# Kernel tuning notes

Measured on AMD Instinct MI355X. Metric: run time of the kernel, lower is better.

The kernel has to match this reference:

```python
import jax, jax.numpy as jnp
import numpy as np

B = 1024       # repertoires (batch)
TCR = 100      # instances (TCRs) per repertoire
FEAT = 15      # feature_num (conv in_channels)
AA = 24        # aa_num (sequence length)
KS = [2, 3, 4, 5, 6, 7]
FN = [3, 3, 3, 2, 2, 1]
NINP = 14      # sum(FN)
EPS = 1e-5     # BatchNorm eps


def sparsemax(z):
    # z: (B, K); sparsemax along axis 1 (Martins & Astudillo 2016)
    K = z.shape[1]
    zs = -jnp.sort(-z, axis=1)               # descending sort
    cs = jnp.cumsum(zs, axis=1)
    k = jnp.arange(1, K + 1, dtype=z.dtype)
    support = 1.0 + k * zs > cs              # (B, K) bool
    ksel = jnp.sum(support, axis=1, keepdims=True).astype(jnp.int32)  # support size
    tau = (jnp.take_along_axis(cs, ksel - 1, axis=1) - 1.0) / ksel.astype(z.dtype)
    return jnp.maximum(z - tau, 0.0)


def setup_inputs() -> dict:
    key = jax.random.key(0)
    ks = jax.random.split(key, 12)
    inp = {"x": jax.random.normal(ks[0], (B, TCR, FEAT, AA), dtype=jnp.float32)}
    for i, (h, f) in enumerate(zip(KS, FN)):
        inp[f"cw{i}"] = jax.random.normal(ks[1 + i], (f, FEAT, h), dtype=jnp.float32) * 0.1
        inp[f"cb{i}"] = jnp.zeros((f,), dtype=jnp.float32)
    inp["fc1_w"] = jax.random.normal(ks[7], (NINP, NINP), dtype=jnp.float32) * 0.2
    inp["fc1_b"] = jnp.zeros((NINP,), dtype=jnp.float32)
    inp["waout_w"] = jax.random.normal(ks[8], (1, NINP), dtype=jnp.float32) * 0.2
    inp["decf_w"] = jax.random.normal(ks[9], (NINP, NINP), dtype=jnp.float32) * 0.2
    inp["decf_b"] = jnp.zeros((NINP,), dtype=jnp.float32)
    inp["bn_g"] = jnp.ones((NINP,), dtype=jnp.float32)
    inp["bn_b"] = jnp.zeros((NINP,), dtype=jnp.float32)
    inp["decs_w"] = jax.random.normal(ks[10], (2, NINP), dtype=jnp.float32) * 0.2
    inp["decs_b"] = jnp.zeros((2,), dtype=jnp.float32)
    return inp


def reference(x, cw0, cb0, cw1, cb1, cw2, cb2, cw3, cb3, cw4, cb4, cw5, cb5,
              fc1_w, fc1_b, waout_w, decf_w, decf_b, bn_g, bn_b, decs_w, decs_b):
    xf = x.reshape(-1, FEAT, AA)  # (B*TCR, 15, 24)
    feats = []
    for w, b in ((cw0, cb0), (cw1, cb1), (cw2, cb2), (cw3, cb3), (cw4, cb4), (cw5, cb5)):
        y = jax.lax.conv_general_dilated(xf, w, (1,), 'VALID',
                                         dimension_numbers=('NCH', 'OIH', 'NCH'))
        y = jax.nn.relu(y + b[None, :, None])
        feats.append(jnp.max(y, axis=-1))  # AdaptiveMaxPool1d(1): global max over length
    out = jnp.concatenate(feats, axis=1).reshape(-1, TCR, NINP)  # (B, TCR, 14)
    # fclayer1 + dropout(eval=identity) + relu; applied per-instance so the
    # torch (TCR, B, .) transpose is equivalent to working in (B, TCR, .)
    h = jax.nn.relu(out @ fc1_w.T + fc1_b)                       # (B, TCR, 14)
    attw = sparsemax(h @ waout_w[0])                             # (B, TCR)
    pooled = jnp.einsum('bt,btd->bd', attw, h)                   # bmm(attw[:,None,:], h)
    z = pooled @ decf_w.T + decf_b                               # decoder_f
    mu = jnp.mean(z, axis=0)                                     # BatchNorm1d (batch stats)
    var = jnp.var(z, axis=0)
    z = jax.nn.relu((z - mu) / jnp.sqrt(var + EPS) * bn_g + bn_b)
    logits = z @ decs_w.T + decs_b                               # decoder_s -> (B, 2)
    return logits, attw
```

## Files before the change

### kernel.cpp

```cpp
#include <hip/hip_runtime.h>

typedef unsigned int  u32;
typedef unsigned short u16;

__device__ __forceinline__ float bf2f(u16 u){
    return __uint_as_float(((u32)u) << 16);
}
__device__ __forceinline__ u16 f2bf(float f){
    u32 x = __float_as_uint(f);
    x += 0x7fffu + ((x >> 16) & 1u);
    return (u16)(x >> 16);
}
__device__ __forceinline__ float ldany(const void* p, int i, bool bf){
    return bf ? bf2f(((const u16*)p)[i]) : ((const float*)p)[i];
}

#define B_      1024
#define TCR_    100
#define NINST   (B_*TCR_)

#define OFF_WL     0
#define OFF_CB     840
#define OFF_FC1W   854
#define OFF_FC1B   1050
#define OFF_WA     1064
#define OFF_DECFW  1078
#define OFF_DECFB  1274
#define OFF_BNG    1288
#define OFF_BNB    1302
#define OFF_DECSW  1316
#define OFF_DECSB  1344
#define NPARAM     1346

__global__ __launch_bounds__(256) void k_pack(
    const void* cw0, const void* cb0, const void* cw1, const void* cb1,
    const void* cw2, const void* cb2, const void* cw3, const void* cb3,
    const void* cw4, const void* cb4, const void* cw5, const void* cb5,
    const void* fc1_w, const void* fc1_b, const void* waout,
    const void* decf_w, const void* decf_b,
    const void* bn_g, const void* bn_b,
    const void* decs_w, const void* decs_b,
    float* __restrict__ wsP)
{
    const int tid = threadIdx.x;
    const bool bf = (((const u16*)bn_g)[0] == 0x3F80u);

    for (int widx = tid; widx < 840; widx += 256){
        float val;
        if (widx < 90)      { int e = widx;       int c=e/6,  rr=e-c*6,  ff=rr/2, j=rr-ff*2; val=ldany(cw0,(ff*15+c)*2+j,bf); }
        else if (widx < 225){ int e = widx - 90;  int c=e/9,  rr=e-c*9,  ff=rr/3, j=rr-ff*3; val=ldany(cw1,(ff*15+c)*3+j,bf); }
        else if (widx < 405){ int e = widx - 225; int c=e/12, rr=e-c*12, ff=rr/4, j=rr-ff*4; val=ldany(cw2,(ff*15+c)*4+j,bf); }
        else if (widx < 555){ int e = widx - 405; int c=e/10, rr=e-c*10, ff=rr/5, j=rr-ff*5; val=ldany(cw3,(ff*15+c)*5+j,bf); }
        else if (widx < 735){ int e = widx - 555; int c=e/12, rr=e-c*12, ff=rr/6, j=rr-ff*6; val=ldany(cw4,(ff*15+c)*6+j,bf); }
        else                { int e = widx - 735; int c=e/7,  j=e-c*7;                        val=ldany(cw5,c*7+j,bf); }
        wsP[OFF_WL + widx] = val;
    }
    for (int i = tid; i < 14; i += 256){
        float bv;
        if (i < 3)       bv = ldany(cb0, i, bf);
        else if (i < 6)  bv = ldany(cb1, i - 3, bf);
        else if (i < 9)  bv = ldany(cb2, i - 6, bf);
        else if (i < 11) bv = ldany(cb3, i - 9, bf);
        else if (i < 13) bv = ldany(cb4, i - 11, bf);
        else             bv = ldany(cb5, 0, bf);
        wsP[OFF_CB    + i] = bv;
        wsP[OFF_FC1B  + i] = ldany(fc1_b,  i, bf);
        wsP[OFF_WA    + i] = ldany(waout,  i, bf);
        wsP[OFF_DECFB + i] = ldany(decf_b, i, bf);
        wsP[OFF_BNG   + i] = ldany(bn_g,   i, bf);
        wsP[OFF_BNB   + i] = ldany(bn_b,   i, bf);
    }
    for (int i = tid; i < 196; i += 256){
        wsP[OFF_FC1W  + i] = ldany(fc1_w,  i, bf);
        wsP[OFF_DECFW + i] = ldany(decf_w, i, bf);
    }
    for (int i = tid; i < 28; i += 256) wsP[OFF_DECSW + i] = ldany(decs_w, i, bf);
    for (int i = tid; i < 2;  i += 256) wsP[OFF_DECSB + i] = ldany(decs_b, i, bf);
}

template<int H, int F, int WOFF, int C0, int C1>
__device__ __forceinline__ void conv_phase(const float* xsf, const float* pl,
                                           float (&acc)[3][23], int lane){
    for (int c = C0; c < C1; ++c){
        float xr[24];
        const float* row = xsf + ((c - C0) * 24) * 65 + lane;
        #pragma unroll
        for (int t = 0; t < 24; ++t) xr[t] = row[t * 65];
        float wv[F * H];
        #pragma unroll
        for (int k = 0; k < F * H; ++k) wv[k] = pl[WOFF + c * F * H + k];
        #pragma unroll
        for (int ff = 0; ff < F; ++ff)
            #pragma unroll
            for (int t = 0; t < 25 - H; ++t)
                #pragma unroll
                for (int j = 0; j < H; ++j)
                    acc[ff][t] = fmaf(wv[ff * H + j], xr[t + j], acc[ff][t]);
    }
}

template<int H, int F, int FB>
__device__ __forceinline__ void conv_epi(float (&acc)[3][23], const float* pl,
                                         float* feats, int lane){
    #pragma unroll
    for (int ff = 0; ff < F; ++ff){
        float m = acc[ff][0];
        #pragma unroll
        for (int t = 1; t < 25 - H; ++t) m = fmaxf(m, acc[ff][t]);
        feats[(FB + ff) * 64 + lane] = fmaxf(m + pl[OFF_CB + FB + ff], 0.0f);
    }
}

__global__ __launch_bounds__(384) void k_conv(
    const void* __restrict__ x, const float* __restrict__ wsP,
    const void* __restrict__ dt,
    float* __restrict__ hbuf, float* __restrict__ sbuf)
{
    __shared__ float xsf[192 * 65];
    __shared__ float pl[1078];
    __shared__ float feats[14 * 64];

    const int tid  = threadIdx.x;
    const int lane = tid & 63;
    const int wvid = tid >> 6;
    const bool bf  = (((const u16*)dt)[0] == 0x3F80u);
    const size_t ibase = (size_t)blockIdx.x * 64;

    for (int i = tid; i < 1078; i += 384) pl[i] = wsP[i];

    float acc[3][23];
    #pragma unroll
    for (int ff = 0; ff < 3; ++ff)
        #pragma unroll
        for (int t = 0; t < 23; ++t) acc[ff][t] = 0.0f;

    if (bf){
        const u32* xp = (const u32*)x;
        #pragma unroll
        for (int it = 0; it < 16; ++it){
            int idx  = it * 384 + tid;
            int inst = idx / 96;
            int kd   = idx - inst * 96;
            u32 v = xp[(ibase + inst) * 180 + kd];
            int k = kd * 2;
            xsf[k * 65 + inst]       = bf2f((u16)(v & 0xffffu));
            xsf[(k + 1) * 65 + inst] = bf2f((u16)(v >> 16));
        }
    } else {
        const float* xp = (const float*)x;
        #pragma unroll
        for (int it = 0; it < 32; ++it){
            int idx  = it * 384 + tid;
            int inst = idx / 192;
            int k    = idx - inst * 192;
            xsf[k * 65 + inst] = xp[(ibase + inst) * 360 + k];
        }
    }
    __syncthreads();
    switch (wvid){
        case 0: conv_phase<2,3,  0, 0,8>(xsf, pl, acc, lane); break;
        case 1: conv_phase<3,3, 90, 0,8>(xsf, pl, acc, lane); break;
        case 2: conv_phase<4,3,225, 0,8>(xsf, pl, acc, lane); break;
        case 3: conv_phase<5,2,405, 0,8>(xsf, pl, acc, lane); break;
        case 4: conv_phase<6,2,555, 0,8>(xsf, pl, acc, lane); break;
        default:conv_phase<7,1,735, 0,8>(xsf, pl, acc, lane); break;
    }
    __syncthreads();
    if (bf){
        const u32* xp = (const u32*)x;
        #pragma unroll
        for (int it = 0; it < 14; ++it){
            int idx  = it * 384 + tid;
            int inst = idx / 84;
            int kd   = idx - inst * 84;
            u32 v = xp[(ibase + inst) * 180 + 96 + kd];
            int k = kd * 2;
            xsf[k * 65 + inst]       = bf2f((u16)(v & 0xffffu));
            xsf[(k + 1) * 65 + inst] = bf2f((u16)(v >> 16));
        }
    } else {
        const float* xp = (const float*)x;
        #pragma unroll
        for (int it = 0; it < 28; ++it){
            int idx  = it * 384 + tid;
            int inst = idx / 168;
            int k    = idx - inst * 168;
            xsf[k * 65 + inst] = xp[(ibase + inst) * 360 + 192 + k];
        }
    }
    __syncthreads();
    switch (wvid){
        case 0: conv_phase<2,3,  0, 8,15>(xsf, pl, acc, lane); break;
        case 1: conv_phase<3,3, 90, 8,15>(xsf, pl, acc, lane); break;
        case 2: conv_phase<4,3,225, 8,15>(xsf, pl, acc, lane); break;
        case 3: conv_phase<5,2,405, 8,15>(xsf, pl, acc, lane); break;
        case 4: conv_phase<6,2,555, 8,15>(xsf, pl, acc, lane); break;
        default:conv_phase<7,1,735, 8,15>(xsf, pl, acc, lane); break;
    }
    switch (wvid){
        case 0: conv_epi<2,3, 0>(acc, pl, feats, lane); break;
        case 1: conv_epi<3,3, 3>(acc, pl, feats, lane); break;
        case 2: conv_epi<4,3, 6>(acc, pl, feats, lane); break;
        case 3: conv_epi<5,2, 9>(acc, pl, feats, lane); break;
        case 4: conv_epi<6,2,11>(acc, pl, feats, lane); break;
        default:conv_epi<7,1,13>(acc, pl, feats, lane); break;
    }
    __syncthreads();

    if (wvid == 0){
        float ft[14];
        #pragma unroll
        for (int j = 0; j < 14; ++j) ft[j] = feats[j * 64 + lane];
        float hv[14];
        #pragma unroll
        for (int i = 0; i < 14; ++i){
            float a = pl[OFF_FC1B + i];
            #pragma unroll
            for (int j = 0; j < 14; ++j) a = fmaf(ft[j], pl[OFF_FC1W + i * 14 + j], a);
            hv[i] = fmaxf(a, 0.0f);
        }
        float sc = 0.0f;
        #pragma unroll
        for (int i = 0; i < 14; ++i) sc = fmaf(hv[i], pl[OFF_WA + i], sc);
        size_t inst = ibase + lane;
        #pragma unroll
        for (int i = 0; i < 14; ++i) hbuf[inst * 14 + i] = hv[i];
        sbuf[inst] = sc;
    }
}

__global__ __launch_bounds__(64) void k_sparse(
    const float* __restrict__ hbuf, const float* __restrict__ sbuf,
    const float* __restrict__ wsP, const void* __restrict__ dt,
    float* __restrict__ zbuf, void* __restrict__ d_out)
{
    const int b    = blockIdx.x;
    const int lane = threadIdx.x;
    const bool bf  = (((const u16*)dt)[0] == 0x3F80u);
    const bool has2 = lane < (TCR_ - 64);

    float z0 = sbuf[b * TCR_ + lane];
    float z1 = has2 ? sbuf[b * TCR_ + 64 + lane] : -1e30f;

    float m = fmaxf(z0, z1);
    #pragma unroll
    for (int o = 32; o; o >>= 1) m = fmaxf(m, __shfl_xor(m, o));

    float lo = m - 1.0f, hi = m;
    for (int it = 0; it < 32; ++it){
        float mid = 0.5f * (lo + hi);
        float s = fmaxf(z0 - mid, 0.0f) + fmaxf(z1 - mid, 0.0f);
        #pragma unroll
        for (int o = 32; o; o >>= 1) s += __shfl_xor(s, o);
        if (s >= 1.0f) lo = mid; else hi = mid;
    }
    float tau = 0.5f * (lo + hi);
    float a0 = fmaxf(z0 - tau, 0.0f);
    float a1 = fmaxf(z1 - tau, 0.0f);

    if (bf){
        u16* aw = (u16*)d_out + 2048;
        aw[b * TCR_ + lane] = f2bf(a0);
        if (has2) aw[b * TCR_ + 64 + lane] = f2bf(a1);
    } else {
        float* aw = (float*)d_out + 2048;
        aw[b * TCR_ + lane] = a0;
        if (has2) aw[b * TCR_ + 64 + lane] = a1;
    }

    float ap[14];
    const float* h0 = hbuf + (size_t)(b * TCR_ + lane) * 14;
    const float* h1 = hbuf + (size_t)(b * TCR_ + 64 + lane) * 14;
    #pragma unroll
    for (int d = 0; d < 14; ++d){
        float v = a0 * h0[d];
        if (has2) v += a1 * h1[d];
        #pragma unroll
        for (int o = 32; o; o >>= 1) v += __shfl_xor(v, o);
        ap[d] = v;
    }
    if (lane < 14){
        float zv = wsP[OFF_DECFB + lane];
        #pragma unroll
        for (int j = 0; j < 14; ++j) zv = fmaf(ap[j], wsP[OFF_DECFW + lane * 14 + j], zv);
        zbuf[b * 14 + lane] = zv;
    }
}

__global__ __launch_bounds__(256) void k_bn(
    const float* __restrict__ zbuf, const float* __restrict__ wsP,
    const void* __restrict__ dt, void* __restrict__ d_out)
{
    __shared__ float part[4][28];
    __shared__ float red[28];
    const int tid  = threadIdx.x;
    const int lane = tid & 63;
    const int w    = tid >> 6;
    const bool bf  = (((const u16*)dt)[0] == 0x3F80u);

    float z[4][14];
    #pragma unroll
    for (int r = 0; r < 4; ++r)
        #pragma unroll
        for (int d = 0; d < 14; ++d) z[r][d] = zbuf[(tid + 256 * r) * 14 + d];

    #pragma unroll
    for (int d = 0; d < 14; ++d){
        float s = 0.0f, q = 0.0f;
        #pragma unroll
        for (int r = 0; r < 4; ++r){ s += z[r][d]; q += z[r][d] * z[r][d]; }
        #pragma unroll
        for (int o = 32; o; o >>= 1){ s += __shfl_xor(s, o); q += __shfl_xor(q, o); }
        if (lane == 0){ part[w][d] = s; part[w][14 + d] = q; }
    }
    __syncthreads();
    if (tid < 28) red[tid] = part[0][tid] + part[1][tid] + part[2][tid] + part[3][tid];
    __syncthreads();

    float mu[14], rs[14];
    #pragma unroll
    for (int d = 0; d < 14; ++d){
        mu[d] = red[d] * (1.0f / 1024.0f);
        float var = red[14 + d] * (1.0f / 1024.0f) - mu[d] * mu[d];
        rs[d] = rsqrtf(var + 1e-5f);
    }
    #pragma unroll
    for (int r = 0; r < 4; ++r){
        float zn[14];
        #pragma unroll
        for (int d = 0; d < 14; ++d)
            zn[d] = fmaxf((z[r][d] - mu[d]) * rs[d] * wsP[OFF_BNG + d] + wsP[OFF_BNB + d], 0.0f);
        #pragma unroll
        for (int c = 0; c < 2; ++c){
            float a = wsP[OFF_DECSB + c];
            #pragma unroll
            for (int d = 0; d < 14; ++d) a = fmaf(zn[d], wsP[OFF_DECSW + c * 14 + d], a);
            if (bf) ((u16*)d_out)[(tid + 256 * r) * 2 + c] = f2bf(a);
            else    ((float*)d_out)[(tid + 256 * r) * 2 + c] = a;
        }
    }
}

extern "C" void kernel_launch(void* const* d_in, const int* in_sizes, int n_in,
                              void* d_out, int out_size, void* d_ws, size_t ws_size,
                              hipStream_t stream)
{
    (void)in_sizes; (void)n_in; (void)out_size; (void)ws_size;
    const void* x     = d_in[0];
    const void* bn_g  = d_in[18];

    float* wsP  = (float*)d_ws;
    float* hbuf = wsP + 2048;
    float* sbuf = hbuf + (size_t)NINST * 14;
    float* zbuf = sbuf + NINST;

    k_pack<<<1, 256, 0, stream>>>(
        d_in[1], d_in[2], d_in[3], d_in[4], d_in[5], d_in[6],
        d_in[7], d_in[8], d_in[9], d_in[10], d_in[11], d_in[12],
        d_in[13], d_in[14], d_in[15], d_in[16], d_in[17],
        d_in[18], d_in[19], d_in[20], d_in[21], wsP);
    k_conv<<<NINST / 64, 384, 0, stream>>>(x, wsP, bn_g, hbuf, sbuf);
    k_sparse<<<B_, 64, 0, stream>>>(hbuf, sbuf, wsP, bn_g, zbuf, d_out);
    k_bn<<<1, 256, 0, stream>>>(zbuf, wsP, bn_g, d_out);
}
```

Baseline: 358.7 us.

## Compute all conv filters per thread from registers, dropping shared-memory staging

The conv kernel drops the 384-thread block that staged 64 instances in LDS and gave each wave one kernel size. Now each thread handles one whole instance: it streams each channel row straight from global memory with vector loads, prefetches the next channel, and evaluates the six filter groups in three paired passes with weights read from global. The h buffer is stored feature-major so both the writes in conv and the reads in sparse are coalesced. This removes LDS traffic, barriers and the wave load imbalance, at the cost of uncoalesced per-thread row loads (each thread reads a contiguous 720/1440-byte row), more register pressure and 64-thread blocks.

```diff
diff --git a/kernel.cpp b/kernel.cpp
--- a/kernel.cpp
+++ b/kernel.cpp
@@ -6,6 +6,8 @@
 __device__ __forceinline__ float bf2f(u16 u){
     return __uint_as_float(((u32)u) << 16);
 }
+__device__ __forceinline__ float lo16(u32 v){ return __uint_as_float(v << 16); }
+__device__ __forceinline__ float hi16(u32 v){ return __uint_as_float(v & 0xffff0000u); }
 __device__ __forceinline__ u16 f2bf(float f){
     u32 x = __float_as_uint(f);
     x += 0x7fffu + ((x >> 16) & 1u);
@@ -30,7 +32,6 @@
 #define OFF_BNB    1302
 #define OFF_DECSW  1316
 #define OFF_DECSB  1344
-#define NPARAM     1346
 
 __global__ __launch_bounds__(256) void k_pack(
     const void* cw0, const void* cb0, const void* cw1, const void* cb1,
@@ -78,159 +79,136 @@
     for (int i = tid; i < 2;  i += 256) wsP[OFF_DECSB + i] = ldany(decs_b, i, bf);
 }
 
-template<int H, int F, int WOFF, int C0, int C1>
-__device__ __forceinline__ void conv_phase(const float* xsf, const float* pl,
-                                           float (&acc)[3][23], int lane){
-    for (int c = C0; c < C1; ++c){
-        float xr[24];
-        const float* row = xsf + ((c - C0) * 24) * 65 + lane;
-        #pragma unroll
-        for (int t = 0; t < 24; ++t) xr[t] = row[t * 65];
-        float wv[F * H];
-        #pragma unroll
-        for (int k = 0; k < F * H; ++k) wv[k] = pl[WOFF + c * F * H + k];
-        #pragma unroll
-        for (int ff = 0; ff < F; ++ff)
+template<int H, int F, int WOFF>
+__device__ __forceinline__ void acc_channel(float (&acc)[F][25 - H], const float* xr,
+                                            const float* __restrict__ wsP, int c){
+    float wv[F * H];
+    const float* wc = wsP + WOFF + c * (F * H);
+    #pragma unroll
+    for (int k = 0; k < F * H; ++k) wv[k] = wc[k];
+    #pragma unroll
+    for (int ff = 0; ff < F; ++ff)
+        #pragma unroll
+        for (int t = 0; t < 25 - H; ++t)
             #pragma unroll
-            for (int t = 0; t < 25 - H; ++t)
-                #pragma unroll
-                for (int j = 0; j < H; ++j)
-                    acc[ff][t] = fmaf(wv[ff * H + j], xr[t + j], acc[ff][t]);
-    }
-}
-
-template<int H, int F, int FB>
-__device__ __forceinline__ void conv_epi(float (&acc)[3][23], const float* pl,
-                                         float* feats, int lane){
+            for (int j = 0; j < H; ++j)
+                acc[ff][t] = fmaf(wv[ff * H + j], xr[t + j], acc[ff][t]);
+}
+
+template<int H, int F, int OF>
+__device__ __forceinline__ void group_max(float (&acc)[F][25 - H],
+                                          const float* __restrict__ wsP, float* feats){
     #pragma unroll
     for (int ff = 0; ff < F; ++ff){
         float m = acc[ff][0];
         #pragma unroll
         for (int t = 1; t < 25 - H; ++t) m = fmaxf(m, acc[ff][t]);
-        feats[(FB + ff) * 64 + lane] = fmaxf(m + pl[OFF_CB + FB + ff], 0.0f);
-    }
-}
-
-__global__ __launch_bounds__(384) void k_conv(
+        feats[OF + ff] = fmaxf(m + wsP[OFF_CB + OF + ff], 0.0f);
+    }
+}
+
+template<bool BF>
+__device__ __forceinline__ void unpackx(const uint4* buf, float* xr){
+    constexpr int NB = BF ? 3 : 6;
+    #pragma unroll
+    for (int i = 0; i < NB; ++i){
+        u32 w0 = buf[i].x, w1 = buf[i].y, w2 = buf[i].z, w3 = buf[i].w;
+        if (BF){
+            xr[i*8+0] = lo16(w0); xr[i*8+1] = hi16(w0);
+            xr[i*8+2] = lo16(w1); xr[i*8+3] = hi16(w1);
+            xr[i*8+4] = lo16(w2); xr[i*8+5] = hi16(w2);
+            xr[i*8+6] = lo16(w3); xr[i*8+7] = hi16(w3);
+        } else {
+            xr[i*4+0] = __uint_as_float(w0); xr[i*4+1] = __uint_as_float(w1);
+            xr[i*4+2] = __uint_as_float(w2); xr[i*4+3] = __uint_as_float(w3);
+        }
+    }
+}
+
+template<bool BF, int HA,int FA,int WA,int OFA, int HB,int FBn,int WB,int OFB>
+__device__ __forceinline__ void conv_pass(const char* xb, const float* __restrict__ wsP,
+                                          float* feats){
+    constexpr int NB = BF ? 3 : 6;
+    constexpr int CS = BF ? 48 : 96;
+    float accA[FA][25 - HA];
+    float accB[FBn][25 - HB];
+    #pragma unroll
+    for (int ff = 0; ff < FA; ++ff)
+        #pragma unroll
+        for (int t = 0; t < 25 - HA; ++t) accA[ff][t] = 0.0f;
+    #pragma unroll
+    for (int ff = 0; ff < FBn; ++ff)
+        #pragma unroll
+        for (int t = 0; t < 25 - HB; ++t) accB[ff][t] = 0.0f;
+
+    uint4 buf[NB];
+    {
+        const uint4* p = (const uint4*)xb;
+        #pragma unroll
+        for (int i = 0; i < NB; ++i) buf[i] = p[i];
+    }
+    #pragma unroll 1
+    for (int c = 0; c < 15; ++c){
+        uint4 nbuf[NB];
+        int cn = (c < 14) ? (c + 1) : 14;
+        const uint4* pn = (const uint4*)(xb + cn * CS);
+        #pragma unroll
+        for (int i = 0; i < NB; ++i) nbuf[i] = pn[i];
+
+        float xr[24];
+        unpackx<BF>(buf, xr);
+        acc_channel<HA, FA, WA>(accA, xr, wsP, c);
+        acc_channel<HB, FBn, WB>(accB, xr, wsP, c);
+
+        #pragma unroll
+        for (int i = 0; i < NB; ++i) buf[i] = nbuf[i];
+    }
+    group_max<HA, FA, OFA>(accA, wsP, feats);
+    group_max<HB, FBn, OFB>(accB, wsP, feats);
+}
+
+template<bool BF>
+__device__ __forceinline__ void conv_body(const void* __restrict__ x,
+                                          const float* __restrict__ wsP,
+                                          float* __restrict__ hbufT,
+                                          float* __restrict__ sbuf){
+    const int inst = blockIdx.x * 64 + threadIdx.x;
+    const char* xb = (const char*)x + (size_t)inst * (BF ? 720 : 1440);
+
+    float feats[14];
+    conv_pass<BF, 2,3,  0, 0,  7,1,735,13>(xb, wsP, feats);
+    conv_pass<BF, 3,3, 90, 3,  6,2,555,11>(xb, wsP, feats);
+    conv_pass<BF, 4,3,225, 6,  5,2,405, 9>(xb, wsP, feats);
+
+    float hv[14];
+    #pragma unroll
+    for (int i = 0; i < 14; ++i){
+        float a = wsP[OFF_FC1B + i];
+        #pragma unroll
+        for (int j = 0; j < 14; ++j) a = fmaf(feats[j], wsP[OFF_FC1W + i * 14 + j], a);
+        hv[i] = fmaxf(a, 0.0f);
+    }
+    float sc = 0.0f;
+    #pragma unroll
+    for (int i = 0; i < 14; ++i) sc = fmaf(hv[i], wsP[OFF_WA + i], sc);
+
+    #pragma unroll
+    for (int d = 0; d < 14; ++d) hbufT[d * NINST + inst] = hv[d];
+    sbuf[inst] = sc;
+}
+
+__global__ __launch_bounds__(64) void k_conv(
     const void* __restrict__ x, const float* __restrict__ wsP,
     const void* __restrict__ dt,
-    float* __restrict__ hbuf, float* __restrict__ sbuf)
-{
-    __shared__ float xsf[192 * 65];
-    __shared__ float pl[1078];
-    __shared__ float feats[14 * 64];
-
-    const int tid  = threadIdx.x;
-    const int lane = tid & 63;
-    const int wvid = tid >> 6;
-    const bool bf  = (((const u16*)dt)[0] == 0x3F80u);
-    const size_t ibase = (size_t)blockIdx.x * 64;
-
-    for (int i = tid; i < 1078; i += 384) pl[i] = wsP[i];
-
-    float acc[3][23];
-    #pragma unroll
-    for (int ff = 0; ff < 3; ++ff)
-        #pragma unroll
-        for (int t = 0; t < 23; ++t) acc[ff][t] = 0.0f;
-
-    if (bf){
-        const u32* xp = (const u32*)x;
-        #pragma unroll
-        for (int it = 0; it < 16; ++it){
-            int idx  = it * 384 + tid;
-            int inst = idx / 96;
-            int kd   = idx - inst * 96;
-            u32 v = xp[(ibase + inst) * 180 + kd];
-            int k = kd * 2;
-            xsf[k * 65 + inst]       = bf2f((u16)(v & 0xffffu));
-            xsf[(k + 1) * 65 + inst] = bf2f((u16)(v >> 16));
-        }
-    } else {
-        const float* xp = (const float*)x;
-        #pragma unroll
-        for (int it = 0; it < 32; ++it){
-            int idx  = it * 384 + tid;
-            int inst = idx / 192;
-            int k    = idx - inst * 192;
-            xsf[k * 65 + inst] = xp[(ibase + inst) * 360 + k];
-        }
-    }
-    __syncthreads();
-    switch (wvid){
-        case 0: conv_phase<2,3,  0, 0,8>(xsf, pl, acc, lane); break;
-        case 1: conv_phase<3,3, 90, 0,8>(xsf, pl, acc, lane); break;
-        case 2: conv_phase<4,3,225, 0,8>(xsf, pl, acc, lane); break;
-        case 3: conv_phase<5,2,405, 0,8>(xsf, pl, acc, lane); break;
-        case 4: conv_phase<6,2,555, 0,8>(xsf, pl, acc, lane); break;
-        default:conv_phase<7,1,735, 0,8>(xsf, pl, acc, lane); break;
-    }
-    __syncthreads();
-    if (bf){
-        const u32* xp = (const u32*)x;
-        #pragma unroll
-        for (int it = 0; it < 14; ++it){
-            int idx  = it * 384 + tid;
-            int inst = idx / 84;
-            int kd   = idx - inst * 84;
-            u32 v = xp[(ibase + inst) * 180 + 96 + kd];
-            int k = kd * 2;
-            xsf[k * 65 + inst]       = bf2f((u16)(v & 0xffffu));
-            xsf[(k + 1) * 65 + inst] = bf2f((u16)(v >> 16));
-        }
-    } else {
-        const float* xp = (const float*)x;
-        #pragma unroll
-        for (int it = 0; it < 28; ++it){
-            int idx  = it * 384 + tid;
-            int inst = idx / 168;
-            int k    = idx - inst * 168;
-            xsf[k * 65 + inst] = xp[(ibase + inst) * 360 + 192 + k];
-        }
-    }
-    __syncthreads();
-    switch (wvid){
-        case 0: conv_phase<2,3,  0, 8,15>(xsf, pl, acc, lane); break;
-        case 1: conv_phase<3,3, 90, 8,15>(xsf, pl, acc, lane); break;
-        case 2: conv_phase<4,3,225, 8,15>(xsf, pl, acc, lane); break;
-        case 3: conv_phase<5,2,405, 8,15>(xsf, pl, acc, lane); break;
-        case 4: conv_phase<6,2,555, 8,15>(xsf, pl, acc, lane); break;
-        default:conv_phase<7,1,735, 8,15>(xsf, pl, acc, lane); break;
-    }
-    switch (wvid){
-        case 0: conv_epi<2,3, 0>(acc, pl, feats, lane); break;
-        case 1: conv_epi<3,3, 3>(acc, pl, feats, lane); break;
-        case 2: conv_epi<4,3, 6>(acc, pl, feats, lane); break;
-        case 3: conv_epi<5,2, 9>(acc, pl, feats, lane); break;
-        case 4: conv_epi<6,2,11>(acc, pl, feats, lane); break;
-        default:conv_epi<7,1,13>(acc, pl, feats, lane); break;
-    }
-    __syncthreads();
-
-    if (wvid == 0){
-        float ft[14];
-        #pragma unroll
-        for (int j = 0; j < 14; ++j) ft[j] = feats[j * 64 + lane];
-        float hv[14];
-        #pragma unroll
-        for (int i = 0; i < 14; ++i){
-            float a = pl[OFF_FC1B + i];
-            #pragma unroll
-            for (int j = 0; j < 14; ++j) a = fmaf(ft[j], pl[OFF_FC1W + i * 14 + j], a);
-            hv[i] = fmaxf(a, 0.0f);
-        }
-        float sc = 0.0f;
-        #pragma unroll
-        for (int i = 0; i < 14; ++i) sc = fmaf(hv[i], pl[OFF_WA + i], sc);
-        size_t inst = ibase + lane;
-        #pragma unroll
-        for (int i = 0; i < 14; ++i) hbuf[inst * 14 + i] = hv[i];
-        sbuf[inst] = sc;
-    }
+    float* __restrict__ hbufT, float* __restrict__ sbuf)
+{
+    const bool bf = (((const u16*)dt)[0] == 0x3F80u);
+    if (bf) conv_body<true >(x, wsP, hbufT, sbuf);
+    else    conv_body<false>(x, wsP, hbufT, sbuf);
 }
 
 __global__ __launch_bounds__(64) void k_sparse(
-    const float* __restrict__ hbuf, const float* __restrict__ sbuf,
+    const float* __restrict__ hbufT, const float* __restrict__ sbuf,
     const float* __restrict__ wsP, const void* __restrict__ dt,
     float* __restrict__ zbuf, void* __restrict__ d_out)
 {
@@ -269,12 +247,10 @@
     }
 
     float ap[14];
-    const float* h0 = hbuf + (size_t)(b * TCR_ + lane) * 14;
-    const float* h1 = hbuf + (size_t)(b * TCR_ + 64 + lane) * 14;
     #pragma unroll
     for (int d = 0; d < 14; ++d){
-        float v = a0 * h0[d];
-        if (has2) v += a1 * h1[d];
+        float v = a0 * hbufT[d * NINST + b * TCR_ + lane];
+        if (has2) v += a1 * hbufT[d * NINST + b * TCR_ + 64 + lane];
         #pragma unroll
         for (int o = 32; o; o >>= 1) v += __shfl_xor(v, o);
         ap[d] = v;
@@ -349,17 +325,17 @@
     const void* x     = d_in[0];
     const void* bn_g  = d_in[18];
 
-    float* wsP  = (float*)d_ws;
-    float* hbuf = wsP + 2048;
-    float* sbuf = hbuf + (size_t)NINST * 14;
-    float* zbuf = sbuf + NINST;
+    float* wsP   = (float*)d_ws;
+    float* hbufT = wsP + 2048;
+    float* sbuf  = hbufT + (size_t)14 * NINST;
+    float* zbuf  = sbuf + NINST;
 
     k_pack<<<1, 256, 0, stream>>>(
         d_in[1], d_in[2], d_in[3], d_in[4], d_in[5], d_in[6],
         d_in[7], d_in[8], d_in[9], d_in[10], d_in[11], d_in[12],
         d_in[13], d_in[14], d_in[15], d_in[16], d_in[17],
         d_in[18], d_in[19], d_in[20], d_in[21], wsP);
-    k_conv<<<NINST / 64, 384, 0, stream>>>(x, wsP, bn_g, hbuf, sbuf);
-    k_sparse<<<B_, 64, 0, stream>>>(hbuf, sbuf, wsP, bn_g, zbuf, d_out);
+    k_conv<<<NINST / 64, 64, 0, stream>>>(x, wsP, bn_g, hbufT, sbuf);
+    k_sparse<<<B_, 64, 0, stream>>>(hbufT, sbuf, wsP, bn_g, zbuf, d_out);
     k_bn<<<1, 256, 0, stream>>>(zbuf, wsP, bn_g, d_out);
 }
```

Result: no change. 359.3 us (+0.2%).
